# Optimization experiments

Hardware: AMD Instinct MI355X
Metric: run time of the kernel (lower is better)

The kernel has to match this reference:

```python
import jax, jax.numpy as jnp
import numpy as np

N_SAMPLES = 256
D_IN = 512
D_HID = 1024


def setup_inputs() -> dict:
    key = jax.random.key(0)
    k1, k2, k3, k4, k5, k6 = jax.random.split(key, 6)
    x1 = jax.random.normal(k1, (N_SAMPLES, D_IN), dtype=jnp.float32)
    x2 = jax.random.normal(k2, (N_SAMPLES, D_IN), dtype=jnp.float32)
    # MLP params with fan-in scaling (realistic init)
    W1 = jax.random.normal(k3, (D_IN, D_HID), dtype=jnp.float32) / np.sqrt(D_IN)
    b1 = jax.random.normal(k4, (D_HID,), dtype=jnp.float32) * 0.01
    W2 = jax.random.normal(k5, (D_HID, 1), dtype=jnp.float32) / np.sqrt(D_HID)
    b2 = jax.random.normal(k6, (1,), dtype=jnp.float32) * 0.01
    return {"x1": x1, "x2": x2, "W1": W1, "b1": b1, "W2": W2, "b2": b2}


def _per_sample_jacobian(params, x):
    """Per-sample grads of scalar network output w.r.t. params, flattened.

    params: (W1, b1, W2, b2); x: [n, d_in]. Returns J: [n, P].
    """
    def f_single(p, xi):  # xi: [d_in] -> scalar (matches squeeze(-1) in torch)
        W1, b1, W2, b2 = p
        h = jax.nn.relu(xi @ W1 + b1)          # [d_hid]
        return (h @ W2 + b2)[0]                # scalar

    grads = jax.vmap(jax.grad(f_single), in_axes=(None, 0))(params, x)
    n = x.shape[0]
    return jnp.concatenate(
        [g.reshape(n, -1) for g in jax.tree_util.tree_leaves(grads)], axis=1
    )


def reference(x1, x2, W1, b1, W2, b2):
    params = (W1, b1, W2, b2)
    J1 = _per_sample_jacobian(params, x1)  # [n, P]
    J2 = _per_sample_jacobian(params, x2)  # [n, P]
    # Empirical NTK: K[i,j] = <grad_i, grad_j> -- single fused GEMM instead of
    # the original O(n^2) autograd.grad loop.
    return J1 @ J2.T                       # [n, n]
```

## Files before the change

kernel.cpp:

```cpp
#include <hip/hip_runtime.h>
#include <hip/hip_bf16.h>

#define NS   256
#define DIN  512
#define DHID 1024

typedef __attribute__((ext_vector_type(8)))  short bf16x8;
typedef __attribute__((ext_vector_type(4)))  float f32x4;
typedef __attribute__((ext_vector_type(16))) float f32x16;

static __device__ __forceinline__ short f2bf(float f) {
    return __builtin_bit_cast(short, __float2bfloat16(f));
}

static __device__ __forceinline__ bf16x8 cvt8(f32x4 a, f32x4 b) {
    bf16x8 r;
    r[0] = f2bf(a[0]); r[1] = f2bf(a[1]); r[2] = f2bf(a[2]); r[3] = f2bf(a[3]);
    r[4] = f2bf(b[0]); r[5] = f2bf(b[1]); r[6] = f2bf(b[2]); r[7] = f2bf(b[3]);
    return r;
}

__global__ __launch_bounds__(256) void ntk_k1(
    const float* __restrict__ x1, const float* __restrict__ x2,
    const float* __restrict__ W1, const float* __restrict__ b1,
    const float* __restrict__ w2,
    short* __restrict__ Hb, short* __restrict__ Gb,
    float* __restrict__ Cws)
{
    const int tid = threadIdx.x;
    const int l   = tid & 63;
    const int w   = tid >> 6;
    const int lc  = l & 31;
    const int hk  = l >> 5;
    const int b   = blockIdx.x;

    __shared__ f32x16 red[4][64];

    if (b < 128) {
        const int m0  = (b >> 3) * 32;
        const int col = (b & 7) * 128 + w * 32 + lc;
        const float* X  = (m0 < NS) ? (x1 + (size_t)m0 * DIN)
                                    : (x2 + (size_t)(m0 - NS) * DIN);
        const float* ap = X + lc * DIN + hk * 8;
        const float* bp = W1 + (size_t)(hk * 8) * DHID + col;

        f32x16 acc = {};
        #pragma unroll 4
        for (int t = 0; t < 32; ++t) {
            const int k0 = t * 16;
            bf16x8 a = cvt8(*(const f32x4*)(ap + k0), *(const f32x4*)(ap + k0 + 4));
            f32x4 b0v, b1v;
            #pragma unroll
            for (int i = 0; i < 4; ++i) b0v[i] = bp[(size_t)(k0 + i) * DHID];
            #pragma unroll
            for (int i = 0; i < 4; ++i) b1v[i] = bp[(size_t)(k0 + 4 + i) * DHID];
            bf16x8 bf = cvt8(b0v, b1v);
            acc = __builtin_amdgcn_mfma_f32_32x32x16_bf16(a, bf, acc, 0, 0, 0);
        }

        const float bbv = b1[col], wwv = w2[col];
        #pragma unroll
        for (int r = 0; r < 16; ++r) {
            const int row = m0 + (r & 3) + 8 * (r >> 2) + 4 * hk;
            float z = acc[r] + bbv;
            Hb[row * DHID + col] = f2bf(z > 0.f ? z   : 0.f);
            Gb[row * DHID + col] = f2bf(z > 0.f ? wwv : 0.f);
        }
    } else {
        const int bb = b - 128;
        const int bi = (bb >> 3) * 32;
        const int bj = (bb & 7) * 32;
        const float* ar = x1 + (bi + lc) * DIN + hk * 8;
        const float* br = x2 + (bj + lc) * DIN + hk * 8;

        f32x16 ac = {};
        #pragma unroll
        for (int q = 0; q < 8; ++q) {
            const int k0 = (w + q * 4) * 16;
            bf16x8 a  = cvt8(*(const f32x4*)(ar + k0), *(const f32x4*)(ar + k0 + 4));
            bf16x8 bv = cvt8(*(const f32x4*)(br + k0), *(const f32x4*)(br + k0 + 4));
            ac = __builtin_amdgcn_mfma_f32_32x32x16_bf16(a, bv, ac, 0, 0, 0);
        }
        red[w][l] = ac;
        __syncthreads();
        if (w == 0) {
            f32x16 c = red[0][l];
            #pragma unroll
            for (int q = 1; q < 4; ++q) c += red[q][l];
            #pragma unroll
            for (int r = 0; r < 16; ++r) {
                const int row = bi + (r & 3) + 8 * (r >> 2) + 4 * hk;
                Cws[row * NS + (bj + lc)] = c[r];
            }
        }
    }
}

__global__ __launch_bounds__(512) void ntk_k2(
    const short* __restrict__ Hb, const short* __restrict__ Gb,
    const float* __restrict__ Cws, float* __restrict__ out)
{
    const int tid = threadIdx.x;
    const int l   = tid & 63;
    const int w   = tid >> 6;
    const int lr  = l & 15;
    const int kg  = l >> 4;
    const int bi  = (blockIdx.x >> 4) * 16;
    const int bj  = (blockIdx.x & 15) * 16;

    __shared__ f32x4 red[2][8][64];

    f32x4 ag = {0.f,0.f,0.f,0.f}, ah = {0.f,0.f,0.f,0.f};

    const short* ga = Gb + (bi + lr) * DHID + kg * 8;
    const short* gb = Gb + (NS + bj + lr) * DHID + kg * 8;
    const short* ha = Hb + (bi + lr) * DHID + kg * 8;
    const short* hb = Hb + (NS + bj + lr) * DHID + kg * 8;

    #pragma unroll
    for (int t = 0; t < 4; ++t) {
        const int k = (w + t * 8) * 32;
        bf16x8 a  = *(const bf16x8*)(ga + k);
        bf16x8 bv = *(const bf16x8*)(gb + k);
        ag = __builtin_amdgcn_mfma_f32_16x16x32_bf16(a, bv, ag, 0, 0, 0);
        bf16x8 a2 = *(const bf16x8*)(ha + k);
        bf16x8 b2 = *(const bf16x8*)(hb + k);
        ah = __builtin_amdgcn_mfma_f32_16x16x32_bf16(a2, b2, ah, 0, 0, 0);
    }

    red[0][w][l] = ag; red[1][w][l] = ah;
    __syncthreads();
    if (w == 0) {
        f32x4 g = red[0][0][l], h = red[1][0][l];
        #pragma unroll
        for (int q = 1; q < 8; ++q) { g += red[0][q][l]; h += red[1][q][l]; }
        #pragma unroll
        for (int r = 0; r < 4; ++r) {
            const int idx = (bi + kg * 4 + r) * NS + (bj + lr);
            out[idx] = (Cws[idx] + 1.f) * g[r] + h[r] + 1.f;
        }
    }
}

extern "C" void kernel_launch(void* const* d_in, const int* in_sizes, int n_in,
                              void* d_out, int out_size, void* d_ws, size_t ws_size,
                              hipStream_t stream) {
    const float* x1 = (const float*)d_in[0];
    const float* x2 = (const float*)d_in[1];
    const float* W1 = (const float*)d_in[2];
    const float* b1 = (const float*)d_in[3];
    const float* w2 = (const float*)d_in[4];

    short* Hb  = (short*)d_ws;
    short* Gb  = Hb + 2 * NS * DHID;
    float* Cws = (float*)(Gb + 2 * NS * DHID);
    float* out = (float*)d_out;

    ntk_k1<<<192, 256, 0, stream>>>(x1, x2, W1, b1, w2, Hb, Gb, Cws);
    ntk_k2<<<256, 512, 0, stream>>>(Hb, Gb, Cws, out);
}
```

Baseline: 22.92 us.

## Merge two kernels into one cooperative kernel with grid-wide sync

Replaces the two-kernel pipeline with a single cooperative launch of 256 blocks that computes the hidden layer (split-K across wave pairs) and then, after a grid sync, computes the x1·x2ᵀ term together with the G and H Gram products in the second phase. This drops the second kernel launch and the Cws workspace round-trip, and redistributes the work over 256 blocks of 256 threads. The cost is a grid-wide barrier, which needs all blocks to be co-resident, and a second phase that uses 4 waves per block instead of 8.

```diff
diff --git a/kernel.cpp b/kernel.cpp
--- a/kernel.cpp
+++ b/kernel.cpp
@@ -1,5 +1,8 @@
 #include <hip/hip_runtime.h>
 #include <hip/hip_bf16.h>
+#include <hip/hip_cooperative_groups.h>
+
+namespace cg = cooperative_groups;
 
 #define NS   256
 #define DIN  512
@@ -20,25 +23,31 @@
     return r;
 }
 
-__global__ __launch_bounds__(256) void ntk_k1(
+__global__ __launch_bounds__(256) void ntk_coop(
     const float* __restrict__ x1, const float* __restrict__ x2,
     const float* __restrict__ W1, const float* __restrict__ b1,
     const float* __restrict__ w2,
     short* __restrict__ Hb, short* __restrict__ Gb,
-    float* __restrict__ Cws)
+    float* __restrict__ out)
 {
     const int tid = threadIdx.x;
     const int l   = tid & 63;
     const int w   = tid >> 6;
-    const int lc  = l & 31;
-    const int hk  = l >> 5;
     const int b   = blockIdx.x;
 
-    __shared__ f32x16 red[4][64];
+    __shared__ __align__(16) char smem[16384];
+    auto red1 = reinterpret_cast<f32x16(*)[2][64]>(smem);
+    auto red2 = reinterpret_cast<f32x4(*)[4][64]>(smem);
 
-    if (b < 128) {
-        const int m0  = (b >> 3) * 32;
-        const int col = (b & 7) * 128 + w * 32 + lc;
+    {
+        const int lc = l & 31;
+        const int hk = l >> 5;
+        const int ct = w >> 1;
+        const int ks = w & 1;
+        const int m0 = (b >> 4) * 32;
+        const int n0 = (b & 15) * 64;
+        const int col = n0 + ct * 32 + lc;
+
         const float* X  = (m0 < NS) ? (x1 + (size_t)m0 * DIN)
                                     : (x2 + (size_t)(m0 - NS) * DIN);
         const float* ap = X + lc * DIN + hk * 8;
@@ -46,7 +55,7 @@
 
         f32x16 acc = {};
         #pragma unroll 4
-        for (int t = 0; t < 32; ++t) {
+        for (int t = ks * 16; t < ks * 16 + 16; ++t) {
             const int k0 = t * 16;
             bf16x8 a = cvt8(*(const f32x4*)(ap + k0), *(const f32x4*)(ap + k0 + 4));
             f32x4 b0v, b1v;
@@ -54,90 +63,68 @@
             for (int i = 0; i < 4; ++i) b0v[i] = bp[(size_t)(k0 + i) * DHID];
             #pragma unroll
             for (int i = 0; i < 4; ++i) b1v[i] = bp[(size_t)(k0 + 4 + i) * DHID];
-            bf16x8 bf = cvt8(b0v, b1v);
-            acc = __builtin_amdgcn_mfma_f32_32x32x16_bf16(a, bf, acc, 0, 0, 0);
+            acc = __builtin_amdgcn_mfma_f32_32x32x16_bf16(a, cvt8(b0v, b1v), acc, 0, 0, 0);
         }
-
-        const float bbv = b1[col], wwv = w2[col];
-        #pragma unroll
-        for (int r = 0; r < 16; ++r) {
-            const int row = m0 + (r & 3) + 8 * (r >> 2) + 4 * hk;
-            float z = acc[r] + bbv;
-            Hb[row * DHID + col] = f2bf(z > 0.f ? z   : 0.f);
-            Gb[row * DHID + col] = f2bf(z > 0.f ? wwv : 0.f);
-        }
-    } else {
-        const int bb = b - 128;
-        const int bi = (bb >> 3) * 32;
-        const int bj = (bb & 7) * 32;
-        const float* ar = x1 + (bi + lc) * DIN + hk * 8;
-        const float* br = x2 + (bj + lc) * DIN + hk * 8;
-
-        f32x16 ac = {};
-        #pragma unroll
-        for (int q = 0; q < 8; ++q) {
-            const int k0 = (w + q * 4) * 16;
-            bf16x8 a  = cvt8(*(const f32x4*)(ar + k0), *(const f32x4*)(ar + k0 + 4));
-            bf16x8 bv = cvt8(*(const f32x4*)(br + k0), *(const f32x4*)(br + k0 + 4));
-            ac = __builtin_amdgcn_mfma_f32_32x32x16_bf16(a, bv, ac, 0, 0, 0);
-        }
-        red[w][l] = ac;
+        red1[ct][ks][l] = acc;
         __syncthreads();
-        if (w == 0) {
-            f32x16 c = red[0][l];
-            #pragma unroll
-            for (int q = 1; q < 4; ++q) c += red[q][l];
+        if (w < 2) {
+            f32x16 s = red1[w][0][l] + red1[w][1][l];
+            const int colw = n0 + w * 32 + lc;
+            const float bbv = b1[colw], wwv = w2[colw];
             #pragma unroll
             for (int r = 0; r < 16; ++r) {
-                const int row = bi + (r & 3) + 8 * (r >> 2) + 4 * hk;
-                Cws[row * NS + (bj + lc)] = c[r];
+                const int row = m0 + (r & 3) + 8 * (r >> 2) + 4 * hk;
+                float z = s[r] + bbv;
+                Hb[row * DHID + colw] = f2bf(z > 0.f ? z   : 0.f);
+                Gb[row * DHID + colw] = f2bf(z > 0.f ? wwv : 0.f);
             }
         }
     }
-}
 
-__global__ __launch_bounds__(512) void ntk_k2(
-    const short* __restrict__ Hb, const short* __restrict__ Gb,
-    const float* __restrict__ Cws, float* __restrict__ out)
-{
-    const int tid = threadIdx.x;
-    const int l   = tid & 63;
-    const int w   = tid >> 6;
-    const int lr  = l & 15;
-    const int kg  = l >> 4;
-    const int bi  = (blockIdx.x >> 4) * 16;
-    const int bj  = (blockIdx.x & 15) * 16;
+    cg::this_grid().sync();
 
-    __shared__ f32x4 red[2][8][64];
+    {
+        const int lr = l & 15;
+        const int kg = l >> 4;
+        const int bi = (b >> 4) * 16;
+        const int bj = (b & 15) * 16;
 
-    f32x4 ag = {0.f,0.f,0.f,0.f}, ah = {0.f,0.f,0.f,0.f};
+        f32x4 ac = {0.f,0.f,0.f,0.f}, ag = {0.f,0.f,0.f,0.f}, ah = {0.f,0.f,0.f,0.f};
 
-    const short* ga = Gb + (bi + lr) * DHID + kg * 8;
-    const short* gb = Gb + (NS + bj + lr) * DHID + kg * 8;
-    const short* ha = Hb + (bi + lr) * DHID + kg * 8;
-    const short* hb = Hb + (NS + bj + lr) * DHID + kg * 8;
+        const float* ar = x1 + (bi + lr) * DIN + kg * 8;
+        const float* br = x2 + (bj + lr) * DIN + kg * 8;
+        #pragma unroll
+        for (int t = 0; t < 4; ++t) {
+            const int k = (w + t * 4) * 32;
+            bf16x8 a  = cvt8(*(const f32x4*)(ar + k), *(const f32x4*)(ar + k + 4));
+            bf16x8 bv = cvt8(*(const f32x4*)(br + k), *(const f32x4*)(br + k + 4));
+            ac = __builtin_amdgcn_mfma_f32_16x16x32_bf16(a, bv, ac, 0, 0, 0);
+        }
+        const short* ga = Gb + (bi + lr) * DHID + kg * 8;
+        const short* gb = Gb + (NS + bj + lr) * DHID + kg * 8;
+        const short* ha = Hb + (bi + lr) * DHID + kg * 8;
+        const short* hb = Hb + (NS + bj + lr) * DHID + kg * 8;
+        #pragma unroll
+        for (int t = 0; t < 8; ++t) {
+            const int k = (w + t * 4) * 32;
+            bf16x8 a  = *(const bf16x8*)(ga + k);
+            bf16x8 bv = *(const bf16x8*)(gb + k);
+            ag = __builtin_amdgcn_mfma_f32_16x16x32_bf16(a, bv, ag, 0, 0, 0);
+            bf16x8 a2 = *(const bf16x8*)(ha + k);
+            bf16x8 b2 = *(const bf16x8*)(hb + k);
+            ah = __builtin_amdgcn_mfma_f32_16x16x32_bf16(a2, b2, ah, 0, 0, 0);
+        }
 
-    #pragma unroll
-    for (int t = 0; t < 4; ++t) {
-        const int k = (w + t * 8) * 32;
-        bf16x8 a  = *(const bf16x8*)(ga + k);
-        bf16x8 bv = *(const bf16x8*)(gb + k);
-        ag = __builtin_amdgcn_mfma_f32_16x16x32_bf16(a, bv, ag, 0, 0, 0);
-        bf16x8 a2 = *(const bf16x8*)(ha + k);
-        bf16x8 b2 = *(const bf16x8*)(hb + k);
-        ah = __builtin_amdgcn_mfma_f32_16x16x32_bf16(a2, b2, ah, 0, 0, 0);
-    }
-
-    red[0][w][l] = ag; red[1][w][l] = ah;
-    __syncthreads();
-    if (w == 0) {
-        f32x4 g = red[0][0][l], h = red[1][0][l];
-        #pragma unroll
-        for (int q = 1; q < 8; ++q) { g += red[0][q][l]; h += red[1][q][l]; }
-        #pragma unroll
-        for (int r = 0; r < 4; ++r) {
-            const int idx = (bi + kg * 4 + r) * NS + (bj + lr);
-            out[idx] = (Cws[idx] + 1.f) * g[r] + h[r] + 1.f;
+        __syncthreads();
+        red2[0][w][l] = ac; red2[1][w][l] = ag; red2[2][w][l] = ah;
+        __syncthreads();
+        if (w == 0) {
+            f32x4 c = red2[0][0][l], g = red2[1][0][l], h = red2[2][0][l];
+            #pragma unroll
+            for (int q = 1; q < 4; ++q) { c += red2[0][q][l]; g += red2[1][q][l]; h += red2[2][q][l]; }
+            #pragma unroll
+            for (int r = 0; r < 4; ++r)
+                out[(bi + kg * 4 + r) * NS + (bj + lr)] = (c[r] + 1.f) * g[r] + h[r] + 1.f;
         }
     }
 }
@@ -153,9 +140,10 @@
 
     short* Hb  = (short*)d_ws;
     short* Gb  = Hb + 2 * NS * DHID;
-    float* Cws = (float*)(Gb + 2 * NS * DHID);
     float* out = (float*)d_out;
 
-    ntk_k1<<<192, 256, 0, stream>>>(x1, x2, W1, b1, w2, Hb, Gb, Cws);
-    ntk_k2<<<256, 512, 0, stream>>>(Hb, Gb, Cws, out);
+    void* args[] = { (void*)&x1, (void*)&x2, (void*)&W1, (void*)&b1,
+                     (void*)&w2, (void*)&Hb, (void*)&Gb, (void*)&out };
+    (void)hipLaunchCooperativeKernel((const void*)ntk_coop, dim3(256), dim3(256),
+                                     args, 0, stream);
 }
```

New measurement: 57.20 us. 150% more time.
